# Performance work log

Measured on AMD Instinct MI355X. Metric: run time of the kernel, lower is better.

## Reference

```python
import jax, jax.numpy as jnp
import numpy as np

# Model dims (match init_kwargs)
B, S, D, H = 2, 1024, 1024, 8
NKV = 1024            # num_key_values = nearest square to 4*D/4 = D -> 32^2
NK = 32               # sqrt(num_key_values) = PK num_keys
NP = 2                # product_keys
DK = D // 16          # PK dim_key
TK = 8                # product_key_topk == final_topk == key_value_pk_topk


def setup_inputs() -> dict:
    key = jax.random.key(0)
    ks = jax.random.split(key, 7)
    std = jnp.float32(0.02)
    return {
        "inputs": jax.random.normal(ks[0], (B, S, D), jnp.float32),
        "Wq": jax.random.normal(ks[1], (D * H, D), jnp.float32) * std,       # to_queries (torch Linear [out,in])
        "Wpk": jax.random.normal(ks[2], (DK * NP * H, D), jnp.float32) * std, # PK.to_queries
        "pk_keys": jax.random.normal(ks[3], (NP, NK, H, DK), jnp.float32) * std,
        "keys_emb": jax.random.normal(ks[4], (NKV * H, D), jnp.float32) * std,
        "values_emb": jax.random.normal(ks[5], (NKV * H, D), jnp.float32) * std,
        "Wo": jax.random.normal(ks[6], (D, D * H), jnp.float32) * std,        # to_out
    }


def reference(inputs, Wq, Wpk, pk_keys, keys_emb, values_emb, Wo):
    b, s, d = inputs.shape
    # queries: per-head dim == d; scale by d**-0.5
    q = (inputs @ Wq.T).reshape(b, s, H, d).transpose(0, 2, 1, 3) * (d ** -0.5)  # [B,H,S,D]

    # ---- PK product-key routing ----
    pq = (inputs @ Wpk.T).reshape(b, s, NP, H, DK)
    sim = jnp.einsum('bsphd,pnhd->pbshn', pq, pk_keys)          # [NP,B,S,H,NK]
    sc, ix = jax.lax.top_k(sim, TK)                             # [NP,B,S,H,TK]
    # combine the two sub-key spaces (strides = [1, NK])
    comb_ix = (ix[0][..., :, None] + ix[1][..., None, :] * NK).reshape(b, s, H, TK * TK)
    comb_sc = (sc[0][..., :, None] + sc[1][..., None, :]).reshape(b, s, H, TK * TK)
    fsc, pki = jax.lax.top_k(comb_sc, TK)                       # final_topk = TK
    fidx = jnp.take_along_axis(comb_ix, pki, axis=-1)           # [B,S,H,TK]
    w = jax.nn.softmax(fsc, axis=-1)                            # softmax_scores=True

    # ---- per-head offset + EmbeddingBag('sum') lookups with per-sample weights ----
    idx = fidx + (jnp.arange(H) * NKV)[None, None, :, None]     # [B,S,H,TK]
    k = jnp.einsum('bshtd,bsht->bhsd', keys_emb[idx], w)        # weighted-sum bag
    v = jnp.einsum('bshtd,bsht->bhsd', values_emb[idx], w)

    # ---- causal attention ----
    att = jnp.einsum('bhqd,bhkd->bhqk', q, k)                   # [B,H,S,S]
    causal = jnp.triu(jnp.ones((s, s), bool), 1)
    att = jnp.where(causal, -jnp.finfo(att.dtype).max, att)
    att = jax.nn.softmax(att, axis=-1)
    out = jnp.einsum('bhqk,bhkd->bqhd', att, v).reshape(b, s, H * d)
    return out @ Wo.T
```

## Files before the change

### kernel.cpp

```cpp
#include <hip/hip_runtime.h>
#include <hip/hip_bf16.h>

#define BB   2
#define SS   1024
#define DD   1024
#define HH   8
#define NPP  2
#define NKK  32
#define DKK  64
#define TKK  8
#define NKV_ 1024

typedef __hip_bfloat16 bf16;
typedef __attribute__((ext_vector_type(8))) short bf16x8;
typedef __attribute__((ext_vector_type(4))) float f32x4;

using u32g = __attribute__((address_space(1))) unsigned int;
using u32l = __attribute__((address_space(3))) unsigned int;

#define GLDS16(g, l) __builtin_amdgcn_global_load_lds((const u32g*)(g), (u32l*)(l), 16, 0, 0)

__device__ inline unsigned short f2b(float f) {
    unsigned x = __float_as_uint(f);
    return (unsigned short)((x + 0x7fffu + ((x >> 16) & 1u)) >> 16);
}
__device__ inline float b2f(unsigned short u) {
    return __uint_as_float(((unsigned)u) << 16);
}

__global__ __launch_bounds__(256) void cvt_bf(const float* __restrict__ src,
                                              bf16* __restrict__ dst, long long n)
{
    long long i = ((long long)blockIdx.x * 256 + threadIdx.x) * 4;
    if (i >= n) return;
    float4 v = *(const float4*)&src[i];
    ushort4 u; u.x = f2b(v.x); u.y = f2b(v.y); u.z = f2b(v.z); u.w = f2b(v.w);
    *(ushort4*)&dst[i] = u;
}

__global__ __launch_bounds__(256) void reduce_split(
    const float* __restrict__ p, float* __restrict__ out,
    long long n, int nsplit, float scale)
{
    long long i = ((long long)blockIdx.x * 256 + threadIdx.x) * 4;
    if (i >= n) return;
    float4 a = *(const float4*)&p[i];
    for (int s = 1; s < nsplit; ++s) {
        float4 b = *(const float4*)&p[i + (long long)s * n];
        a.x += b.x; a.y += b.y; a.z += b.z; a.w += b.w;
    }
    a.x *= scale; a.y *= scale; a.z *= scale; a.w *= scale;
    *(float4*)&out[i] = a;
}

template<typename TC, int CAUSAL>
__global__ __launch_bounds__(256) void mgemm(
    const bf16* __restrict__ A, const bf16* __restrict__ B, TC* __restrict__ C,
    int K, int lda, int ldb, int ldc,
    long long sAb, long long sAh, long long sBb, long long sBh,
    long long sCb, long long sCh, int zH, float scale)
{
    int gx = gridDim.x, gy = gridDim.y;
    int nwg = gx * gy * gridDim.z;
    int hw  = (blockIdx.z * gy + blockIdx.y) * gx + blockIdx.x;
    int w   = (hw & 7) * (nwg >> 3) + (hw >> 3);
    int bx  = w % gx;
    int rem = w / gx;
    int by  = rem % gy;
    int z   = rem / gy;

    int zb = z / zH, zh = z % zH;
    A += (long long)zb * sAb + (long long)zh * sAh;
    B += (long long)zb * sBb + (long long)zh * sBh;
    C += (long long)zb * sCb + (long long)zh * sCh;

    int row0 = by * 128, col0 = bx * 128;
    if (CAUSAL == 1 && col0 > row0 + 127) return;
    int Klim = (CAUSAL == 2) ? min(K, row0 + 128) : K;

    __shared__ short sh[16384];
    short* As = sh;
    short* Bs = sh + 8192;

    int tid = threadIdx.x, wave = tid >> 6, lane = tid & 63;
    int wr = wave >> 1, wc = wave & 1;
    int lr = lane & 15, lg = lane >> 4;

    f32x4 zero = {0.f, 0.f, 0.f, 0.f};
    f32x4 acc[4][4];
    #pragma unroll
    for (int m = 0; m < 4; ++m)
        #pragma unroll
        for (int n = 0; n < 4; ++n) acc[m][n] = zero;

    int srow = wave * 32 + (lane >> 3);
    int scol = ((lane & 7) ^ (lane >> 3)) * 8;
    int fo = (lg ^ (lr & 7)) * 8;

    for (int k0 = 0; k0 < Klim; k0 += 64) {
        const bf16* Ak = A + (long long)(row0 + srow) * lda + k0 + scol;
        const bf16* Bk = B + (long long)(col0 + srow) * ldb + k0 + scol;
        #pragma unroll
        for (int i = 0; i < 4; ++i) {
            GLDS16(Ak + (long long)i * 8 * lda, &As[(wave * 32 + i * 8) * 64]);
            GLDS16(Bk + (long long)i * 8 * ldb, &Bs[(wave * 32 + i * 8) * 64]);
        }
        asm volatile("s_waitcnt vmcnt(0)" ::: "memory");
        __syncthreads();

        #pragma unroll
        for (int kk = 0; kk < 2; ++kk) {
            bf16x8 af[4], bfr[4];
            #pragma unroll
            for (int m = 0; m < 4; ++m)
                af[m] = *(const bf16x8*)&As[(wr * 64 + m * 16 + lr) * 64 + (fo ^ (kk * 32))];
            #pragma unroll
            for (int n = 0; n < 4; ++n)
                bfr[n] = *(const bf16x8*)&Bs[(wc * 64 + n * 16 + lr) * 64 + (fo ^ (kk * 32))];
            #pragma unroll
            for (int m = 0; m < 4; ++m)
                #pragma unroll
                for (int n = 0; n < 4; ++n)
                    acc[m][n] = __builtin_amdgcn_mfma_f32_16x16x32_bf16(
                        af[m], bfr[n], acc[m][n], 0, 0, 0);
        }
        __syncthreads();
    }

    if constexpr (sizeof(TC) == 2) {
        short* cs = &sh[wave * 4096];
        #pragma unroll
        for (int m = 0; m < 4; ++m)
            #pragma unroll
            for (int n = 0; n < 4; ++n)
                #pragma unroll
                for (int r = 0; r < 4; ++r) {
                    int rl = m * 16 + lg * 4 + r;
                    int cc = (n * 2 + (lr >> 3)) ^ (rl & 7);
                    cs[rl * 64 + cc * 8 + (lr & 7)] =
                        (short)f2b(scale * acc[m][n][r]);
                }
        #pragma unroll
        for (int i = 0; i < 8; ++i) {
            int rl = i * 8 + (lane >> 3);
            int ch = (lane & 7) ^ (lane >> 3);
            bf16x8 v = *(const bf16x8*)&cs[rl * 64 + ch * 8];
            *(bf16x8*)&C[(long long)(row0 + wr * 64 + rl) * ldc
                         + col0 + wc * 64 + (lane & 7) * 8] = v;
        }
    } else {
        #pragma unroll
        for (int m = 0; m < 4; ++m) {
            int row = row0 + wr * 64 + m * 16 + lg * 4;
            #pragma unroll
            for (int n = 0; n < 4; ++n) {
                int col = col0 + wc * 64 + n * 16 + lr;
                #pragma unroll
                for (int r = 0; r < 4; ++r)
                    C[(long long)(row + r) * ldc + col] = scale * acc[m][n][r];
            }
        }
    }
}

#define TILE 64
#define KT   16
#define LPAD 4
__global__ __launch_bounds__(256) void pq_fix(
    const float* __restrict__ A, const float* __restrict__ Bm, float* __restrict__ C)
{
    long long zo = (long long)blockIdx.z * 1024 * 1024;
    A += zo; C += zo;
    int col0 = blockIdx.x * TILE;
    __shared__ float As[KT][TILE + LPAD];
    __shared__ float Bs[KT][TILE + LPAD];
    int tid = threadIdx.x, tx = tid % 16, ty = tid / 16;
    float acc[4][4] = {{0.f}};
    int lr = tid / 4, lk = (tid % 4) * 4;

    for (int k0 = 0; k0 < 1024; k0 += KT) {
        float4 va = *(const float4*)&A[(long long)lr * 1024 + k0 + lk];
        As[lk + 0][lr] = va.x; As[lk + 1][lr] = va.y;
        As[lk + 2][lr] = va.z; As[lk + 3][lr] = va.w;
        float4 vb = *(const float4*)&Bm[(long long)(col0 + lr) * 1024 + k0 + lk];
        Bs[lk + 0][lr] = vb.x; Bs[lk + 1][lr] = vb.y;
        Bs[lk + 2][lr] = vb.z; Bs[lk + 3][lr] = vb.w;
        __syncthreads();
        #pragma unroll
        for (int kk = 0; kk < KT; ++kk) {
            float a[4], b[4];
            #pragma unroll
            for (int i = 0; i < 4; ++i) a[i] = As[kk][ty * 4 + i];
            #pragma unroll
            for (int j = 0; j < 4; ++j) b[j] = Bs[kk][tx * 4 + j];
            #pragma unroll
            for (int i = 0; i < 4; ++i)
                #pragma unroll
                for (int j = 0; j < 4; ++j)
                    acc[i][j] = fmaf(a[i], b[j], acc[i][j]);
        }
        __syncthreads();
    }
    #pragma unroll
    for (int i = 0; i < 4; ++i)
        *(float4*)&C[(long long)(ty * 4 + i) * 1024 + col0 + tx * 4] =
            make_float4(acc[i][0], acc[i][1], acc[i][2], acc[i][3]);
}

__device__ inline unsigned ord_f32(float f) {
    unsigned u = __float_as_uint(f);
    return (u >> 31) ? ~u : (u | 0x80000000u);
}
__device__ inline float unord_f32(unsigned m) {
    unsigned u = (m >> 31) ? (m ^ 0x80000000u) : ~m;
    return __uint_as_float(u);
}

__global__ __launch_bounds__(256) void pk_route(
    const float* __restrict__ pq, const float* __restrict__ pkk,
    float* __restrict__ wts, int* __restrict__ idxs)
{
    int bid  = blockIdx.x * 4 + (threadIdx.x >> 6);
    int lane = threadIdx.x & 63;
    int h    = bid % HH;
    long long bs = bid / HH;
    int p = lane >> 5, n = lane & 31;

    const float* pv = pq  + (bs * NPP + p) * (HH * DKK) + h * DKK;
    const float* kv = pkk + ((long long)(p * NKK + n) * HH + h) * DKK;
    float s = 0.f;
    #pragma unroll
    for (int d = 0; d < DKK; d += 4) {
        float4 q4 = *(const float4*)&pv[d];
        float4 k4 = *(const float4*)&kv[d];
        s = fmaf(q4.x, k4.x, fmaf(q4.y, k4.y, fmaf(q4.z, k4.z, fmaf(q4.w, k4.w, s))));
    }

    unsigned long long key =
        ((unsigned long long)ord_f32(s) << 32) | (unsigned)(31 - n);
    #pragma unroll
    for (int k = 2; k <= 32; k <<= 1) {
        #pragma unroll
        for (int j = k >> 1; j > 0; j >>= 1) {
            unsigned long long other = __shfl_xor(key, j);
            bool keep_big = ((n & k) == 0) == ((n & j) == 0);
            key = (keep_big == (other > key)) ? other : key;
        }
    }
    float keepv = unord_f32((unsigned)(key >> 32));
    int   keepn = 31 - (int)(key & 31);

    int ci = lane >> 3, cj = lane & 7;
    float c0 = __shfl(keepv, ci);
    float c1 = __shfl(keepv, 32 + cj);
    float cv = c0 + c1;

    unsigned long long k2 =
        ((unsigned long long)ord_f32(cv) << 32) | (unsigned)(63 - lane);
    #pragma unroll
    for (int k = 2; k <= 64; k <<= 1) {
        #pragma unroll
        for (int j = k >> 1; j > 0; j >>= 1) {
            unsigned long long other = __shfl_xor(k2, j);
            bool keep_big = ((lane & k) == 0) == ((lane & j) == 0);
            k2 = (keep_big == (other > k2)) ? other : k2;
        }
    }
    int   f   = 63 - (int)(k2 & 63);
    float fsv = unord_f32((unsigned)(k2 >> 32));
    int n0 = __shfl(keepn, f >> 3);
    int n1 = __shfl(keepn, 32 + (f & 7));
    int fsi = n0 + n1 * NKK;

    float m0 = __shfl(fsv, 0);
    float e = (lane < TKK) ? expf(fsv - m0) : 0.f;
    float sum = e;
    #pragma unroll
    for (int off = 1; off < 8; off <<= 1) sum += __shfl_xor(sum, off);
    if (lane < TKK) {
        wts[(long long)bid * TKK + lane]  = e / sum;
        idxs[(long long)bid * TKK + lane] = fsi + h * NKV_;
    }
}

__global__ __launch_bounds__(256) void gather_kv(
    const bf16* __restrict__ keb, const bf16* __restrict__ veb,
    const float* __restrict__ wts, const int* __restrict__ idxs,
    bf16* __restrict__ kb, bf16* __restrict__ vsd)
{
    int bid = blockIdx.x;
    int h = bid % HH;
    int bs = bid / HH;
    int b = bs / SS, s = bs % SS;

    float w[TKK]; long long rb[TKK];
    #pragma unroll
    for (int t = 0; t < TKK; ++t) {
        w[t]  = wts[(long long)bid * TKK + t];
        rb[t] = (long long)idxs[(long long)bid * TKK + t] * DD;
    }
    int c0 = threadIdx.x * 4;
    long long off = (((long long)b * HH + h) * SS + s) * DD + c0;

    ushort4 ld[TKK];
    #pragma unroll
    for (int t = 0; t < TKK; ++t) ld[t] = *(const ushort4*)&keb[rb[t] + c0];
    float4 a = {0.f, 0.f, 0.f, 0.f};
    #pragma unroll
    for (int t = 0; t < TKK; ++t) {
        a.x += w[t] * b2f(ld[t].x); a.y += w[t] * b2f(ld[t].y);
        a.z += w[t] * b2f(ld[t].z); a.w += w[t] * b2f(ld[t].w);
    }
    ushort4 o; o.x = f2b(a.x); o.y = f2b(a.y); o.z = f2b(a.z); o.w = f2b(a.w);
    *(ushort4*)&kb[off] = o;

    #pragma unroll
    for (int t = 0; t < TKK; ++t) ld[t] = *(const ushort4*)&veb[rb[t] + c0];
    a = make_float4(0.f, 0.f, 0.f, 0.f);
    #pragma unroll
    for (int t = 0; t < TKK; ++t) {
        a.x += w[t] * b2f(ld[t].x); a.y += w[t] * b2f(ld[t].y);
        a.z += w[t] * b2f(ld[t].z); a.w += w[t] * b2f(ld[t].w);
    }
    o.x = f2b(a.x); o.y = f2b(a.y); o.z = f2b(a.z); o.w = f2b(a.w);
    *(ushort4*)&vsd[off] = o;
}

__global__ __launch_bounds__(256) void tr64ip(bf16* __restrict__ m)
{
    __shared__ unsigned short La[64][65];
    __shared__ unsigned short Lb[64][65];
    unsigned short* M = (unsigned short*)m + (long long)blockIdx.y * SS * DD;

    int p = blockIdx.x, ti = 0;
    while (p >= 16 - ti) { p -= 16 - ti; ++ti; }
    int tj = ti + p;
    int a0r = ti * 64, a0c = tj * 64;
    int b0r = tj * 64, b0c = ti * 64;

    int r = threadIdx.x / 16, c4 = (threadIdx.x % 16) * 4;
    #pragma unroll
    for (int i = 0; i < 4; ++i) {
        int sr = r + i * 16;
        ushort4 va = *(const ushort4*)&M[(long long)(a0r + sr) * DD + a0c + c4];
        La[sr][c4] = va.x; La[sr][c4+1] = va.y; La[sr][c4+2] = va.z; La[sr][c4+3] = va.w;
        if (ti != tj) {
            ushort4 vb = *(const ushort4*)&M[(long long)(b0r + sr) * DD + b0c + c4];
            Lb[sr][c4] = vb.x; Lb[sr][c4+1] = vb.y; Lb[sr][c4+2] = vb.z; Lb[sr][c4+3] = vb.w;
        }
    }
    __syncthreads();
    #pragma unroll
    for (int i = 0; i < 4; ++i) {
        int dr = r + i * 16;
        ushort4 va;
        va.x = La[c4][dr]; va.y = La[c4+1][dr]; va.z = La[c4+2][dr]; va.w = La[c4+3][dr];
        *(ushort4*)&M[(long long)(b0r + dr) * DD + b0c + c4] = va;
        if (ti != tj) {
            ushort4 vb;
            vb.x = Lb[c4][dr]; vb.y = Lb[c4+1][dr]; vb.z = Lb[c4+2][dr]; vb.w = Lb[c4+3][dr];
            *(ushort4*)&M[(long long)(a0r + dr) * DD + a0c + c4] = vb;
        }
    }
}

__global__ __launch_bounds__(256) void softmax_causal_bf(bf16* __restrict__ sc)
{
    int r  = blockIdx.x;
    int sq = r % SS;
    unsigned short* row = (unsigned short*)(sc + (long long)r * SS);
    int t = threadIdx.x;
    int nvalid = sq + 1;
    int wlim = ((sq >> 7) + 1) << 7;

    float v[4];
    float lm = -INFINITY;
    #pragma unroll
    for (int i = 0; i < 4; ++i) {
        int j = t + i * 256;
        v[i] = (j < nvalid) ? b2f(row[j]) : -INFINITY;
        lm = fmaxf(lm, v[i]);
    }
    __shared__ float red[256];
    red[t] = lm; __syncthreads();
    for (int o = 128; o > 0; o >>= 1) {
        if (t < o) red[t] = fmaxf(red[t], red[t + o]);
        __syncthreads();
    }
    float m = red[0];
    __syncthreads();

    float e[4], ls = 0.f;
    #pragma unroll
    for (int i = 0; i < 4; ++i) {
        int j = t + i * 256;
        e[i] = (j < nvalid) ? expf(v[i] - m) : 0.f;
        ls += e[i];
    }
    red[t] = ls; __syncthreads();
    for (int o = 128; o > 0; o >>= 1) {
        if (t < o) red[t] += red[t + o];
        __syncthreads();
    }
    float inv = 1.f / red[0];
    #pragma unroll
    for (int i = 0; i < 4; ++i) {
        int j = t + i * 256;
        if (j < wlim) row[j] = f2b(e[i] * inv);
    }
}

extern "C" void kernel_launch(void* const* d_in, const int* in_sizes, int n_in,
                              void* d_out, int out_size, void* d_ws, size_t ws_size,
                              hipStream_t stream)
{
    const float* inputs     = (const float*)d_in[0];
    const float* Wq         = (const float*)d_in[1];
    const float* Wpk        = (const float*)d_in[2];
    const float* pk_keys    = (const float*)d_in[3];
    const float* keys_emb   = (const float*)d_in[4];
    const float* values_emb = (const float*)d_in[5];
    const float* Wo         = (const float*)d_in[6];
    float* out = (float*)d_out;

    const long long MB = 1LL << 20;
    char* base = (char*)d_ws;
    bf16* kb  = (bf16*)(base);
    float* spl = (float*)base;
    bf16* qc  = (bf16*)(base + 32*MB);
    bf16* vt  = (bf16*)(base + 64*MB);
    char* screg = base + 96*MB;
    bf16* scb = (bf16*)screg;
    float* pqb = (float*)screg;
    bf16* Wpkb = (bf16*)(screg + 8*MB);
    bf16* Wqb  = (bf16*)(screg + 10*MB);
    bf16* xb   = (bf16*)(screg + 26*MB);
    bf16* keb  = (bf16*)screg;
    bf16* veb  = (bf16*)(screg + 16*MB);
    bf16* Wob  = (bf16*)screg;
    float* wtb = (float*)(base + 128*MB);
    int*   ixb = (int*)(base + 128*MB + (512<<10));
    size_t needed = (size_t)(129*MB);
    if (ws_size < needed) return;

    const long long SLAB = (long long)SS * HH * DD;
    const long long SD   = (long long)SS * DD;
    const long long OUTN = 2048LL * 1024;

    cvt_bf<<<dim3(2048), 256, 0, stream>>>(inputs, xb, 2097152LL);
    cvt_bf<<<dim3(1024), 256, 0, stream>>>(Wpk, Wpkb, 1048576LL);
    cvt_bf<<<dim3(8192), 256, 0, stream>>>(Wq, Wqb, 8388608LL);

    mgemm<float, 0><<<dim3(8, 16, 2), 256, 0, stream>>>(
        xb, Wpkb, spl, 512, 1024, 1024, 1024,
        512, 0, 512, 0, OUTN, 0, 1, 1.0f);
    reduce_split<<<dim3(2048), 256, 0, stream>>>(spl, pqb, OUTN, 2, 1.0f);

    pq_fix<<<dim3(16, 1, 2), 256, 0, stream>>>(inputs, Wpk, pqb);

    pk_route<<<dim3(BB * SS * HH / 4), 256, 0, stream>>>(pqb, pk_keys, wtb, ixb);

    mgemm<bf16, 0><<<dim3(64, 16, 1), 256, 0, stream>>>(
        xb, Wqb, qc, 1024, 1024, 1024, 8192,
        0, 0, 0, 0, 0, 0, 1, 0.03125f);

    cvt_bf<<<dim3(8192), 256, 0, stream>>>(keys_emb, keb, 8388608LL);
    cvt_bf<<<dim3(8192), 256, 0, stream>>>(values_emb, veb, 8388608LL);

    gather_kv<<<dim3(BB * SS * HH), 256, 0, stream>>>(
        keb, veb, wtb, ixb, kb, vt);

    tr64ip<<<dim3(136, BB * HH), 256, 0, stream>>>(vt);

    mgemm<bf16, 1><<<dim3(8, 8, BB * HH), 256, 0, stream>>>(
        qc, kb, scb, 1024, 8192, 1024, 1024,
        SLAB, (long long)DD, (long long)HH * SD, SD,
        (long long)HH * SS * SS, (long long)SS * SS, HH, 1.0f);

    softmax_causal_bf<<<dim3(BB * HH * SS), 256, 0, stream>>>(scb);

    mgemm<bf16, 2><<<dim3(8, 8, BB * HH), 256, 0, stream>>>(
        scb, vt, qc, 1024, 1024, 1024, 8192,
        (long long)HH * SS * SS, (long long)SS * SS,
        (long long)HH * SD, SD,
        SLAB, (long long)DD, HH, 1.0f);

    cvt_bf<<<dim3(8192), 256, 0, stream>>>(Wo, Wob, 8388608LL);

    mgemm<float, 0><<<dim3(8, 16, 4), 256, 0, stream>>>(
        qc, Wob, spl, 2048, 8192, 8192, 1024,
        2048, 0, 2048, 0, OUTN, 0, 1, 1.0f);
    reduce_split<<<dim3(2048), 256, 0, stream>>>(spl, out, OUTN, 4, 1.0f);
}
```

Measured before the change: 402.9 us.

## Group GEMM tile order, split-K the pq fix GEMM, and wave-per-row softmax

```diff
diff --git a/kernel.cpp b/kernel.cpp
--- a/kernel.cpp
+++ b/kernel.cpp
@@ -53,7 +53,7 @@
     *(float4*)&out[i] = a;
 }
 
-template<typename TC, int CAUSAL>
+template<typename TC, int CAUSAL, int GROUP>
 __global__ __launch_bounds__(256) void mgemm(
     const bf16* __restrict__ A, const bf16* __restrict__ B, TC* __restrict__ C,
     int K, int lda, int ldb, int ldc,
@@ -64,10 +64,10 @@
     int nwg = gx * gy * gridDim.z;
     int hw  = (blockIdx.z * gy + blockIdx.y) * gx + blockIdx.x;
     int w   = (hw & 7) * (nwg >> 3) + (hw >> 3);
-    int bx  = w % gx;
-    int rem = w / gx;
-    int by  = rem % gy;
-    int z   = rem / gy;
+    int z  = w / (gx * gy);
+    int r  = w % (gx * gy);
+    int bx = (r / (gy * GROUP)) * GROUP + (r % GROUP);
+    int by = (r / GROUP) % gy;
 
     int zb = z / zH, zh = z % zH;
     A += (long long)zb * sAb + (long long)zh * sAh;
@@ -134,11 +134,11 @@
             #pragma unroll
             for (int n = 0; n < 4; ++n)
                 #pragma unroll
-                for (int r = 0; r < 4; ++r) {
-                    int rl = m * 16 + lg * 4 + r;
+                for (int r2 = 0; r2 < 4; ++r2) {
+                    int rl = m * 16 + lg * 4 + r2;
                     int cc = (n * 2 + (lr >> 3)) ^ (rl & 7);
                     cs[rl * 64 + cc * 8 + (lr & 7)] =
-                        (short)f2b(scale * acc[m][n][r]);
+                        (short)f2b(scale * acc[m][n][r2]);
                 }
         #pragma unroll
         for (int i = 0; i < 8; ++i) {
@@ -156,8 +156,8 @@
             for (int n = 0; n < 4; ++n) {
                 int col = col0 + wc * 64 + n * 16 + lr;
                 #pragma unroll
-                for (int r = 0; r < 4; ++r)
-                    C[(long long)(row + r) * ldc + col] = scale * acc[m][n][r];
+                for (int r2 = 0; r2 < 4; ++r2)
+                    C[(long long)(row + r2) * ldc + col] = scale * acc[m][n][r2];
             }
         }
     }
@@ -167,18 +167,19 @@
 #define KT   16
 #define LPAD 4
 __global__ __launch_bounds__(256) void pq_fix(
-    const float* __restrict__ A, const float* __restrict__ Bm, float* __restrict__ C)
+    const float* __restrict__ A, const float* __restrict__ Bm, float* __restrict__ P)
 {
     long long zo = (long long)blockIdx.z * 1024 * 1024;
-    A += zo; C += zo;
+    A += zo;
     int col0 = blockIdx.x * TILE;
+    int kbase = blockIdx.y * 256;
     __shared__ float As[KT][TILE + LPAD];
     __shared__ float Bs[KT][TILE + LPAD];
     int tid = threadIdx.x, tx = tid % 16, ty = tid / 16;
     float acc[4][4] = {{0.f}};
     int lr = tid / 4, lk = (tid % 4) * 4;
 
-    for (int k0 = 0; k0 < 1024; k0 += KT) {
+    for (int k0 = kbase; k0 < kbase + 256; k0 += KT) {
         float4 va = *(const float4*)&A[(long long)lr * 1024 + k0 + lk];
         As[lk + 0][lr] = va.x; As[lk + 1][lr] = va.y;
         As[lk + 2][lr] = va.z; As[lk + 3][lr] = va.w;
@@ -201,10 +202,26 @@
         }
         __syncthreads();
     }
+    long long base = ((long long)(blockIdx.y * 2 + blockIdx.z) * 64) * 1024;
     #pragma unroll
     for (int i = 0; i < 4; ++i)
-        *(float4*)&C[(long long)(ty * 4 + i) * 1024 + col0 + tx * 4] =
+        *(float4*)&P[base + (long long)(ty * 4 + i) * 1024 + col0 + tx * 4] =
             make_float4(acc[i][0], acc[i][1], acc[i][2], acc[i][3]);
+}
+
+__global__ __launch_bounds__(256) void pq_fix_red(
+    const float* __restrict__ P, float* __restrict__ pqb)
+{
+    long long i4 = ((long long)blockIdx.x * 256 + threadIdx.x) * 4;
+    if (i4 >= 131072) return;
+    float4 a = *(const float4*)&P[i4];
+    #pragma unroll
+    for (int sp = 1; sp < 4; ++sp) {
+        float4 b = *(const float4*)&P[(long long)sp * 131072 + i4];
+        a.x += b.x; a.y += b.y; a.z += b.z; a.w += b.w;
+    }
+    long long z = i4 >> 16, rem = i4 & 65535;
+    *(float4*)&pqb[z * 1048576 + rem] = a;
 }
 
 __device__ inline unsigned ord_f32(float f) {
@@ -364,49 +381,49 @@
     }
 }
 
-__global__ __launch_bounds__(256) void softmax_causal_bf(bf16* __restrict__ sc)
-{
-    int r  = blockIdx.x;
-    int sq = r % SS;
+__global__ __launch_bounds__(256) void softmax_rows(bf16* __restrict__ sc)
+{
+    int r    = blockIdx.x * 4 + (threadIdx.x >> 6);
+    int lane = threadIdx.x & 63;
+    int sq   = r % SS;
     unsigned short* row = (unsigned short*)(sc + (long long)r * SS);
-    int t = threadIdx.x;
     int nvalid = sq + 1;
     int wlim = ((sq >> 7) + 1) << 7;
-
-    float v[4];
-    float lm = -INFINITY;
-    #pragma unroll
-    for (int i = 0; i < 4; ++i) {
-        int j = t + i * 256;
-        v[i] = (j < nvalid) ? b2f(row[j]) : -INFINITY;
-        lm = fmaxf(lm, v[i]);
-    }
-    __shared__ float red[256];
-    red[t] = lm; __syncthreads();
-    for (int o = 128; o > 0; o >>= 1) {
-        if (t < o) red[t] = fmaxf(red[t], red[t + o]);
-        __syncthreads();
-    }
-    float m = red[0];
-    __syncthreads();
-
-    float e[4], ls = 0.f;
-    #pragma unroll
-    for (int i = 0; i < 4; ++i) {
-        int j = t + i * 256;
-        e[i] = (j < nvalid) ? expf(v[i] - m) : 0.f;
+    int base = lane * 16;
+
+    uint4 u0 = *(const uint4*)&row[base];
+    uint4 u1 = *(const uint4*)&row[base + 8];
+    unsigned uw[8] = {u0.x, u0.y, u0.z, u0.w, u1.x, u1.y, u1.z, u1.w};
+
+    float v[16];
+    float m = -INFINITY;
+    #pragma unroll
+    for (int i = 0; i < 8; ++i) {
+        int j0 = base + i * 2;
+        v[i*2]   = (j0     < nvalid) ? __uint_as_float(uw[i] << 16)          : -INFINITY;
+        v[i*2+1] = (j0 + 1 < nvalid) ? __uint_as_float(uw[i] & 0xffff0000u) : -INFINITY;
+        m = fmaxf(m, fmaxf(v[i*2], v[i*2+1]));
+    }
+    #pragma unroll
+    for (int off = 1; off < 64; off <<= 1) m = fmaxf(m, __shfl_xor(m, off));
+
+    float e[16], ls = 0.f;
+    #pragma unroll
+    for (int i = 0; i < 16; ++i) {
+        e[i] = (base + i < nvalid) ? expf(v[i] - m) : 0.f;
         ls += e[i];
     }
-    red[t] = ls; __syncthreads();
-    for (int o = 128; o > 0; o >>= 1) {
-        if (t < o) red[t] += red[t + o];
-        __syncthreads();
-    }
-    float inv = 1.f / red[0];
-    #pragma unroll
-    for (int i = 0; i < 4; ++i) {
-        int j = t + i * 256;
-        if (j < wlim) row[j] = f2b(e[i] * inv);
+    #pragma unroll
+    for (int off = 1; off < 64; off <<= 1) ls += __shfl_xor(ls, off);
+    float inv = 1.f / ls;
+
+    if (base < wlim) {
+        unsigned ow[8];
+        #pragma unroll
+        for (int i = 0; i < 8; ++i)
+            ow[i] = (unsigned)f2b(e[i*2] * inv) | ((unsigned)f2b(e[i*2+1] * inv) << 16);
+        *(uint4*)&row[base]     = make_uint4(ow[0], ow[1], ow[2], ow[3]);
+        *(uint4*)&row[base + 8] = make_uint4(ow[4], ow[5], ow[6], ow[7]);
     }
 }
 
@@ -451,16 +468,17 @@
     cvt_bf<<<dim3(1024), 256, 0, stream>>>(Wpk, Wpkb, 1048576LL);
     cvt_bf<<<dim3(8192), 256, 0, stream>>>(Wq, Wqb, 8388608LL);
 
-    mgemm<float, 0><<<dim3(8, 16, 2), 256, 0, stream>>>(
+    mgemm<float, 0, 1><<<dim3(8, 16, 2), 256, 0, stream>>>(
         xb, Wpkb, spl, 512, 1024, 1024, 1024,
         512, 0, 512, 0, OUTN, 0, 1, 1.0f);
     reduce_split<<<dim3(2048), 256, 0, stream>>>(spl, pqb, OUTN, 2, 1.0f);
 
-    pq_fix<<<dim3(16, 1, 2), 256, 0, stream>>>(inputs, Wpk, pqb);
+    pq_fix<<<dim3(16, 4, 2), 256, 0, stream>>>(inputs, Wpk, spl);
+    pq_fix_red<<<dim3(128), 256, 0, stream>>>(spl, pqb);
 
     pk_route<<<dim3(BB * SS * HH / 4), 256, 0, stream>>>(pqb, pk_keys, wtb, ixb);
 
-    mgemm<bf16, 0><<<dim3(64, 16, 1), 256, 0, stream>>>(
+    mgemm<bf16, 0, 8><<<dim3(64, 16, 1), 256, 0, stream>>>(
         xb, Wqb, qc, 1024, 1024, 1024, 8192,
         0, 0, 0, 0, 0, 0, 1, 0.03125f);
 
@@ -472,14 +490,14 @@
 
     tr64ip<<<dim3(136, BB * HH), 256, 0, stream>>>(vt);
 
-    mgemm<bf16, 1><<<dim3(8, 8, BB * HH), 256, 0, stream>>>(
+    mgemm<bf16, 1, 1><<<dim3(8, 8, BB * HH), 256, 0, stream>>>(
         qc, kb, scb, 1024, 8192, 1024, 1024,
         SLAB, (long long)DD, (long long)HH * SD, SD,
         (long long)HH * SS * SS, (long long)SS * SS, HH, 1.0f);
 
-    softmax_causal_bf<<<dim3(BB * HH * SS), 256, 0, stream>>>(scb);
-
-    mgemm<bf16, 2><<<dim3(8, 8, BB * HH), 256, 0, stream>>>(
+    softmax_rows<<<dim3(BB * HH * SS / 4), 256, 0, stream>>>(scb);
+
+    mgemm<bf16, 2, 1><<<dim3(8, 8, BB * HH), 256, 0, stream>>>(
         scb, vt, qc, 1024, 1024, 1024, 8192,
         (long long)HH * SS * SS, (long long)SS * SS,
         (long long)HH * SD, SD,
@@ -487,7 +505,7 @@
 
     cvt_bf<<<dim3(8192), 256, 0, stream>>>(Wo, Wob, 8388608LL);
 
-    mgemm<float, 0><<<dim3(8, 16, 4), 256, 0, stream>>>(
+    mgemm<float, 0, 1><<<dim3(8, 16, 4), 256, 0, stream>>>(
         qc, Wob, spl, 2048, 8192, 8192, 1024,
         2048, 0, 2048, 0, OUTN, 0, 1, 1.0f);
     reduce_split<<<dim3(2048), 256, 0, stream>>>(spl, out, OUTN, 4, 1.0f);
```

Result: faster. 360.1 us (-10.6%).
